# Optimization experiments

Hardware: AMD Instinct MI355X
Metric: run time of the kernel (lower is better)

Reference implementation:

```python
import jax, jax.numpy as jnp
import numpy as np

H = 32  # hidden size


def _lstm_layer(x_sbi, w_ih, w_hh, b_ih, b_hh):
    # x_sbi: [S, B, in]; w_ih: [4H, in]; w_hh: [4H, H] (torch gate order i,f,g,o)
    S, B, _ = x_sbi.shape
    # precompute input projections for all timesteps: [S, B, 4H]
    xg = jnp.einsum('sbi,gi->sbg', x_sbi, w_ih) + (b_ih + b_hh)

    def step(carry, xg_t):
        h, c = carry
        gates = xg_t + h @ w_hh.T  # [B, 4H]
        i, f, g, o = jnp.split(gates, 4, axis=-1)
        i = jax.nn.sigmoid(i)
        f = jax.nn.sigmoid(f)
        g = jnp.tanh(g)
        o = jax.nn.sigmoid(o)
        c = f * c + i * g
        h = o * jnp.tanh(c)
        return (h, c), h

    h0 = jnp.zeros((B, H), x_sbi.dtype)
    c0 = jnp.zeros((B, H), x_sbi.dtype)
    (h_last, _), hs = jax.lax.scan(step, (h0, c0), xg)
    return hs, h_last  # hs: [S, B, H]


def setup_inputs() -> dict:
    key = jax.random.key(0)
    ks = jax.random.split(key, 12)
    B, S = 4096, 512
    s = 1.0 / np.sqrt(H)  # torch default uniform(-1/sqrt(H), 1/sqrt(H))
    u = lambda k, shape: jax.random.uniform(k, shape, jnp.float32, -s, s)
    return {
        'x': jax.random.normal(ks[0], (B, S, 1), jnp.float32),
        'w_ih0': u(ks[1], (4 * H, 1)),
        'w_hh0': u(ks[2], (4 * H, H)),
        'b_ih0': u(ks[3], (4 * H,)),
        'b_hh0': u(ks[4], (4 * H,)),
        'w_ih1': u(ks[5], (4 * H, H)),
        'w_hh1': u(ks[6], (4 * H, H)),
        'b_ih1': u(ks[7], (4 * H,)),
        'b_hh1': u(ks[8], (4 * H,)),
        'fc1_w': u(ks[9], (16, H)),
        'fc1_b': u(ks[9], (16,)),
        'fc2_w': u(ks[10], (1, 16)),
        'fc2_b': u(ks[11], (1,)),
    }


def reference(x, w_ih0, w_hh0, b_ih0, b_hh0, w_ih1, w_hh1, b_ih1, b_hh1,
              fc1_w, fc1_b, fc2_w, fc2_b):
    x_sbi = jnp.swapaxes(x, 0, 1)  # [S, B, 1]
    hs1, _ = _lstm_layer(x_sbi, w_ih0, w_hh0, b_ih0, b_hh0)
    _, h_last = _lstm_layer(hs1, w_ih1, w_hh1, b_ih1, b_hh1)  # last timestep of layer 2
    y = h_last @ fc1_w.T + fc1_b
    y = jnp.where(y >= 0, y, 0.2 * y)  # leaky_relu(0.2)
    y = y @ fc2_w.T + fc2_b
    return y  # [B, 1]
```

## Files before the change

### kernel.cpp

```cpp
#include <hip/hip_runtime.h>

#define H 32
#define SEQ 512
#define BM 16
#define NTHREADS 512
#define HSTRIDE 40

typedef _Float16 half8 __attribute__((ext_vector_type(8)));
typedef __attribute__((ext_vector_type(4))) float f32x4;

#define L2E 1.44269504088896340736f

__device__ __forceinline__ float rcp_(float x)  { return __builtin_amdgcn_rcpf(x); }
__device__ __forceinline__ float exp2_(float x) { return __builtin_amdgcn_exp2f(x); }
#define MFMA16(A, B, C) __builtin_amdgcn_mfma_f32_16x16x32_f16((A), (B), (C), 0, 0, 0)

__global__ __launch_bounds__(NTHREADS, 2) void lstm_kernel(
    const float* __restrict__ x,
    const float* __restrict__ w_ih0,
    const float* __restrict__ w_hh0,
    const float* __restrict__ b_ih0, const float* __restrict__ b_hh0,
    const float* __restrict__ w_ih1,
    const float* __restrict__ w_hh1,
    const float* __restrict__ b_ih1, const float* __restrict__ b_hh1,
    const float* __restrict__ fc1_w,
    const float* __restrict__ fc1_b,
    const float* __restrict__ fc2_w,
    const float* __restrict__ fc2_b,
    float* __restrict__ out)
{
    __shared__ __align__(16) float    xbufT[SEQ * BM];
    __shared__ __align__(16) _Float16 h1s[2][BM * HSTRIDE];
    __shared__ __align__(16) _Float16 h2s[2][BM * HSTRIDE];
    __shared__ __align__(16) float    h2f[BM * 33];
    __shared__ __align__(16) float    yb[BM * 17];

    const int tid  = threadIdx.x;
    const int lane = tid & 63;
    const int wv   = tid >> 6;
    const int c    = lane & 15;
    const int q    = lane >> 4;
    const int r0   = blockIdx.x * BM;

    {
        const int row = tid >> 5;
        const int s0  = (tid & 31) * 16;
        const float* xr = x + (size_t)(r0 + row) * SEQ + s0;
        #pragma unroll
        for (int i = 0; i < 16; i += 4) {
            float4 v = *(const float4*)&xr[i];
            xbufT[(s0 + i + 0) * BM + row] = v.x;
            xbufT[(s0 + i + 1) * BM + row] = v.y;
            xbufT[(s0 + i + 2) * BM + row] = v.z;
            xbufT[(s0 + i + 3) * BM + row] = v.w;
        }
    }
    for (int i = tid; i < BM * HSTRIDE; i += NTHREADS) {
        h1s[0][i] = (_Float16)0.f; h1s[1][i] = (_Float16)0.f;
        h2s[0][i] = (_Float16)0.f; h2s[1][i] = (_Float16)0.f;
    }

    const float gsc[4] = { -L2E, -L2E, 2.f * L2E, -L2E };
    const int worig = (c & 3) * H + 4 * wv + (c >> 2);
    const float wsc = gsc[c & 3];
    const int kb = 8 * q;
    half8 w0, wih, whh;
    {
        const float* p = &w_hh0[worig * H + kb];
        #pragma unroll
        for (int j = 0; j < 8; ++j) w0[j]  = (_Float16)(p[j] * wsc);
        p = &w_ih1[worig * H + kb];
        #pragma unroll
        for (int j = 0; j < 8; ++j) wih[j] = (_Float16)(p[j] * wsc);
        p = &w_hh1[worig * H + kb];
        #pragma unroll
        for (int j = 0; j < 8; ++j) whh[j] = (_Float16)(p[j] * wsc);
    }

    const int m = c;
    const int u = 4 * wv + q;
    f32x4 bias1v, bias2v;
    float wx[4];
    #pragma unroll
    for (int g = 0; g < 4; ++g) {
        bias1v[g] = (b_ih0[g * H + u] + b_hh0[g * H + u]) * gsc[g];
        bias2v[g] = (b_ih1[g * H + u] + b_hh1[g * H + u]) * gsc[g];
        wx[g]     = w_ih0[g * H + u] * gsc[g];
    }
    float c1 = 0.f, c2 = 0.f, h2last = 0.f;

    const int fofs  = c * HSTRIDE + kb;
    const int whofs = m * HSTRIDE + u;

    __syncthreads();

    auto cell = [&](const f32x4& g, float& cst) -> float {
        float ei = exp2_(g[0]), ef = exp2_(g[1]), eg = exp2_(g[2]), eo = exp2_(g[3]);
        float A  = 1.f + ei, F = 1.f + ef;
        float Gp = eg + 1.f, Gm = eg - 1.f;
        float t1 = A * Gp;
        float num = fmaf(cst, t1, Gm * F);
        float cn  = num * rcp_(F * t1);
        cst = cn;
        float ec = exp2_(fminf(cn * (2.f * L2E), 80.f));
        return (ec - 1.f) * rcp_((1.f + eo) * (ec + 1.f));
    };

    half8 a1prev = {};
    auto do_step = [&](const _Float16* __restrict__ h1r, const _Float16* __restrict__ h2r,
                       _Float16* __restrict__ h1w, _Float16* __restrict__ h2w,
                       int t, bool e1, bool e2) {
        half8 a1  = *(const half8*)(h1r + fofs);
        half8 a2o = *(const half8*)(h2r + fofs);
        if (e1) {
            float xv = xbufT[t * BM + m];
            f32x4 g1 = MFMA16(w0, a1, bias1v);
            #pragma unroll
            for (int j = 0; j < 4; ++j) g1[j] = fmaf(xv, wx[j], g1[j]);
            float h1v = cell(g1, c1);
            h1w[whofs] = (_Float16)h1v;
        }
        if (e2) {
            f32x4 g2 = MFMA16(whh, a2o, MFMA16(wih, a1prev, bias2v));
            float h2v = cell(g2, c2);
            h2last = h2v;
            h2w[whofs] = (_Float16)h2v;
        }
        a1prev = a1;
        __syncthreads();
    };

    do_step(h1s[1], h2s[1], h1s[0], h2s[0], 0, true, false);
    do_step(h1s[0], h2s[0], h1s[1], h2s[1], 1, true, false);
    for (int tt = 0; tt < 255; ++tt) {
        int t = 2 + 2 * tt;
        do_step(h1s[1], h2s[1], h1s[0], h2s[0], t,     true, true);
        do_step(h1s[0], h2s[0], h1s[1], h2s[1], t + 1, true, true);
    }
    do_step(h1s[1], h2s[1], h1s[0], h2s[0], 512, false, true);
    do_step(h1s[0], h2s[0], h1s[1], h2s[1], 513, false, true);

    h2f[m * 33 + u] = h2last;
    __syncthreads();
    if (tid < BM * 16) {
        int rr = tid >> 4, j = tid & 15;
        float acc = fc1_b[j];
        #pragma unroll
        for (int k = 0; k < H; ++k) acc += fc1_w[j * H + k] * h2f[rr * 33 + k];
        acc = acc >= 0.f ? acc : 0.2f * acc;
        yb[rr * 17 + j] = acc * fc2_w[j];
    }
    __syncthreads();
    if (tid < BM) {
        float acc = fc2_b[0];
        #pragma unroll
        for (int j = 0; j < 16; ++j) acc += yb[tid * 17 + j];
        out[r0 + tid] = acc;
    }
}

extern "C" void kernel_launch(void* const* d_in, const int* in_sizes, int n_in,
                              void* d_out, int out_size, void* d_ws, size_t ws_size,
                              hipStream_t stream) {
    const float* x     = (const float*)d_in[0];
    const float* w_ih0 = (const float*)d_in[1];
    const float* w_hh0 = (const float*)d_in[2];
    const float* b_ih0 = (const float*)d_in[3];
    const float* b_hh0 = (const float*)d_in[4];
    const float* w_ih1 = (const float*)d_in[5];
    const float* w_hh1 = (const float*)d_in[6];
    const float* b_ih1 = (const float*)d_in[7];
    const float* b_hh1 = (const float*)d_in[8];
    const float* fc1_w = (const float*)d_in[9];
    const float* fc1_b = (const float*)d_in[10];
    const float* fc2_w = (const float*)d_in[11];
    const float* fc2_b = (const float*)d_in[12];
    float* out = (float*)d_out;

    const int B = in_sizes[0] / SEQ;
    hipLaunchKernelGGL(lstm_kernel, dim3(B / BM), dim3(NTHREADS), 0, stream,
                       x, w_ih0, w_hh0, b_ih0, b_hh0, w_ih1, w_hh1, b_ih1, b_hh1,
                       fc1_w, fc1_b, fc2_w, fc2_b, out);
}
```

Measured before the change: 258.9 us.

## Split LSTM layers across separate wave groups with 4-deep h1 ring buffer

Doubles the block to 1024 threads and assigns layer 1 and layer 2 to separate sets of 8 waves, so each wave runs one cell per step instead of both. The layer-1 hidden state moves to a 4-entry LDS ring so layer 2 can read a lagged copy. The aim is to shorten the serial per-step critical path and raise parallelism per CU. In exchange, the larger block makes each barrier cover more waves, and the doubled thread count with a different occupancy bound may reduce register headroom.

```diff
diff --git a/kernel.cpp b/kernel.cpp
--- a/kernel.cpp
+++ b/kernel.cpp
@@ -3,7 +3,7 @@
 #define H 32
 #define SEQ 512
 #define BM 16
-#define NTHREADS 512
+#define NTHREADS 1024
 #define HSTRIDE 40
 
 typedef _Float16 half8 __attribute__((ext_vector_type(8)));
@@ -15,7 +15,19 @@
 __device__ __forceinline__ float exp2_(float x) { return __builtin_amdgcn_exp2f(x); }
 #define MFMA16(A, B, C) __builtin_amdgcn_mfma_f32_16x16x32_f16((A), (B), (C), 0, 0, 0)
 
-__global__ __launch_bounds__(NTHREADS, 2) void lstm_kernel(
+__device__ __forceinline__ float cell(const f32x4& g, float& cst) {
+    float ei = exp2_(g[0]), ef = exp2_(g[1]), eg = exp2_(g[2]), eo = exp2_(g[3]);
+    float A  = 1.f + ei, F = 1.f + ef;
+    float Gp = eg + 1.f, Gm = eg - 1.f;
+    float t1 = A * Gp;
+    float num = fmaf(cst, t1, Gm * F);
+    float cn  = num * rcp_(F * t1);
+    cst = cn;
+    float ec = exp2_(fminf(cn * (2.f * L2E), 80.f));
+    return (ec - 1.f) * rcp_((1.f + eo) * (ec + 1.f));
+}
+
+__global__ __launch_bounds__(NTHREADS, 4) void lstm_kernel(
     const float* __restrict__ x,
     const float* __restrict__ w_ih0,
     const float* __restrict__ w_hh0,
@@ -30,7 +42,7 @@
     float* __restrict__ out)
 {
     __shared__ __align__(16) float    xbufT[SEQ * BM];
-    __shared__ __align__(16) _Float16 h1s[2][BM * HSTRIDE];
+    __shared__ __align__(16) _Float16 h1s[4][BM * HSTRIDE];
     __shared__ __align__(16) _Float16 h2s[2][BM * HSTRIDE];
     __shared__ __align__(16) float    h2f[BM * 33];
     __shared__ __align__(16) float    yb[BM * 17];
@@ -38,16 +50,18 @@
     const int tid  = threadIdx.x;
     const int lane = tid & 63;
     const int wv   = tid >> 6;
+    const int role = wv >> 3;
+    const int w    = wv & 7;
     const int c    = lane & 15;
     const int q    = lane >> 4;
     const int r0   = blockIdx.x * BM;
 
     {
-        const int row = tid >> 5;
-        const int s0  = (tid & 31) * 16;
+        const int row = tid >> 6;
+        const int s0  = (tid & 63) * 8;
         const float* xr = x + (size_t)(r0 + row) * SEQ + s0;
         #pragma unroll
-        for (int i = 0; i < 16; i += 4) {
+        for (int i = 0; i < 8; i += 4) {
             float4 v = *(const float4*)&xr[i];
             xbufT[(s0 + i + 0) * BM + row] = v.x;
             xbufT[(s0 + i + 1) * BM + row] = v.y;
@@ -55,92 +69,79 @@
             xbufT[(s0 + i + 3) * BM + row] = v.w;
         }
     }
-    for (int i = tid; i < BM * HSTRIDE; i += NTHREADS) {
-        h1s[0][i] = (_Float16)0.f; h1s[1][i] = (_Float16)0.f;
-        h2s[0][i] = (_Float16)0.f; h2s[1][i] = (_Float16)0.f;
+    for (int i = tid; i < 4 * BM * HSTRIDE; i += NTHREADS) ((_Float16*)h1s)[i] = (_Float16)0.f;
+    for (int i = tid; i < 2 * BM * HSTRIDE; i += NTHREADS) ((_Float16*)h2s)[i] = (_Float16)0.f;
+
+    const float gsc[4] = { -L2E, -L2E, 2.f * L2E, -L2E };
+    const int worig = (c & 3) * H + 4 * w + (c >> 2);
+    const float wsc = gsc[c & 3];
+    const int kb = 8 * q;
+    const int m = c;
+    const int u = 4 * w + q;
+
+    half8 wa = {}, wb = {};
+    f32x4 biasv;
+    float wx0 = 0.f, wx1 = 0.f, wx2 = 0.f, wx3 = 0.f;
+    if (role == 0) {
+        const float* p = &w_hh0[worig * H + kb];
+        #pragma unroll
+        for (int j = 0; j < 8; ++j) wa[j] = (_Float16)(p[j] * wsc);
+        #pragma unroll
+        for (int g = 0; g < 4; ++g) biasv[g] = (b_ih0[g * H + u] + b_hh0[g * H + u]) * gsc[g];
+        wx0 = w_ih0[0 * H + u] * gsc[0];
+        wx1 = w_ih0[1 * H + u] * gsc[1];
+        wx2 = w_ih0[2 * H + u] * gsc[2];
+        wx3 = w_ih0[3 * H + u] * gsc[3];
+    } else {
+        const float* p = &w_ih1[worig * H + kb];
+        #pragma unroll
+        for (int j = 0; j < 8; ++j) wa[j] = (_Float16)(p[j] * wsc);
+        p = &w_hh1[worig * H + kb];
+        #pragma unroll
+        for (int j = 0; j < 8; ++j) wb[j] = (_Float16)(p[j] * wsc);
+        #pragma unroll
+        for (int g = 0; g < 4; ++g) biasv[g] = (b_ih1[g * H + u] + b_hh1[g * H + u]) * gsc[g];
     }
 
-    const float gsc[4] = { -L2E, -L2E, 2.f * L2E, -L2E };
-    const int worig = (c & 3) * H + 4 * wv + (c >> 2);
-    const float wsc = gsc[c & 3];
-    const int kb = 8 * q;
-    half8 w0, wih, whh;
-    {
-        const float* p = &w_hh0[worig * H + kb];
-        #pragma unroll
-        for (int j = 0; j < 8; ++j) w0[j]  = (_Float16)(p[j] * wsc);
-        p = &w_ih1[worig * H + kb];
-        #pragma unroll
-        for (int j = 0; j < 8; ++j) wih[j] = (_Float16)(p[j] * wsc);
-        p = &w_hh1[worig * H + kb];
-        #pragma unroll
-        for (int j = 0; j < 8; ++j) whh[j] = (_Float16)(p[j] * wsc);
-    }
-
-    const int m = c;
-    const int u = 4 * wv + q;
-    f32x4 bias1v, bias2v;
-    float wx[4];
-    #pragma unroll
-    for (int g = 0; g < 4; ++g) {
-        bias1v[g] = (b_ih0[g * H + u] + b_hh0[g * H + u]) * gsc[g];
-        bias2v[g] = (b_ih1[g * H + u] + b_hh1[g * H + u]) * gsc[g];
-        wx[g]     = w_ih0[g * H + u] * gsc[g];
-    }
-    float c1 = 0.f, c2 = 0.f, h2last = 0.f;
+    float cst = 0.f;
+    float hlast = 0.f;
 
     const int fofs  = c * HSTRIDE + kb;
     const int whofs = m * HSTRIDE + u;
 
     __syncthreads();
 
-    auto cell = [&](const f32x4& g, float& cst) -> float {
-        float ei = exp2_(g[0]), ef = exp2_(g[1]), eg = exp2_(g[2]), eo = exp2_(g[3]);
-        float A  = 1.f + ei, F = 1.f + ef;
-        float Gp = eg + 1.f, Gm = eg - 1.f;
-        float t1 = A * Gp;
-        float num = fmaf(cst, t1, Gm * F);
-        float cn  = num * rcp_(F * t1);
-        cst = cn;
-        float ec = exp2_(fminf(cn * (2.f * L2E), 80.f));
-        return (ec - 1.f) * rcp_((1.f + eo) * (ec + 1.f));
-    };
+    for (int tb = 0; tb < 516; tb += 4) {
+        #pragma unroll
+        for (int p = 0; p < 4; ++p) {
+            const int t = tb + p;
+            if (role == 0) {
+                if (t < 512) {
+                    half8 a1 = *(const half8*)(&h1s[(p + 3) & 3][0] + fofs);
+                    float xv = xbufT[t * BM + m];
+                    f32x4 g1 = MFMA16(wa, a1, biasv);
+                    g1[0] = fmaf(xv, wx0, g1[0]);
+                    g1[1] = fmaf(xv, wx1, g1[1]);
+                    g1[2] = fmaf(xv, wx2, g1[2]);
+                    g1[3] = fmaf(xv, wx3, g1[3]);
+                    float hv = cell(g1, cst);
+                    h1s[p][whofs] = (_Float16)hv;
+                }
+            } else {
+                if (t >= 2 && t < 514) {
+                    half8 a1L = *(const half8*)(&h1s[(p + 2) & 3][0] + fofs);
+                    half8 a2  = *(const half8*)(&h2s[(p + 1) & 1][0] + fofs);
+                    f32x4 g2 = MFMA16(wb, a2, MFMA16(wa, a1L, biasv));
+                    float hv = cell(g2, cst);
+                    hlast = hv;
+                    h2s[p & 1][whofs] = (_Float16)hv;
+                }
+            }
+            __syncthreads();
+        }
+    }
 
-    half8 a1prev = {};
-    auto do_step = [&](const _Float16* __restrict__ h1r, const _Float16* __restrict__ h2r,
-                       _Float16* __restrict__ h1w, _Float16* __restrict__ h2w,
-                       int t, bool e1, bool e2) {
-        half8 a1  = *(const half8*)(h1r + fofs);
-        half8 a2o = *(const half8*)(h2r + fofs);
-        if (e1) {
-            float xv = xbufT[t * BM + m];
-            f32x4 g1 = MFMA16(w0, a1, bias1v);
-            #pragma unroll
-            for (int j = 0; j < 4; ++j) g1[j] = fmaf(xv, wx[j], g1[j]);
-            float h1v = cell(g1, c1);
-            h1w[whofs] = (_Float16)h1v;
-        }
-        if (e2) {
-            f32x4 g2 = MFMA16(whh, a2o, MFMA16(wih, a1prev, bias2v));
-            float h2v = cell(g2, c2);
-            h2last = h2v;
-            h2w[whofs] = (_Float16)h2v;
-        }
-        a1prev = a1;
-        __syncthreads();
-    };
-
-    do_step(h1s[1], h2s[1], h1s[0], h2s[0], 0, true, false);
-    do_step(h1s[0], h2s[0], h1s[1], h2s[1], 1, true, false);
-    for (int tt = 0; tt < 255; ++tt) {
-        int t = 2 + 2 * tt;
-        do_step(h1s[1], h2s[1], h1s[0], h2s[0], t,     true, true);
-        do_step(h1s[0], h2s[0], h1s[1], h2s[1], t + 1, true, true);
-    }
-    do_step(h1s[1], h2s[1], h1s[0], h2s[0], 512, false, true);
-    do_step(h1s[0], h2s[0], h1s[1], h2s[1], 513, false, true);
-
-    h2f[m * 33 + u] = h2last;
+    if (role == 1) h2f[m * 33 + u] = hlast;
     __syncthreads();
     if (tid < BM * 16) {
         int rr = tid >> 4, j = tid & 15;
```

Result: slower. 274.6 us (+6.1%).
